# Optimization experiments

Hardware: AMD Instinct MI355X
Metric: run time of the kernel (lower is better)

## Reference

```python
import jax, jax.numpy as jnp
import numpy as np

N_NODES = 50000
N_EDGES = 800000
N_GRAPHS = 1000
D_NODE = 92
D_EDGE = 41
D_HID = 128
D_OUT = 1


def _glorot(key, shape):
    fan_in, fan_out = shape[1], shape[0]
    lim = jnp.sqrt(6.0 / (fan_in + fan_out))
    return jax.random.uniform(key, shape, jnp.float32, -lim, lim)


def setup_inputs() -> dict:
    key = jax.random.key(0)
    ks = jax.random.split(key, 16)
    x = jax.random.normal(ks[0], (N_NODES, D_NODE), jnp.float32)
    edge_index = jax.random.randint(ks[1], (2, N_EDGES), 0, N_NODES, jnp.int64)
    edge_attr = jax.random.uniform(ks[2], (N_EDGES, D_EDGE), jnp.float32)
    batch = jnp.sort(jax.random.randint(ks[3], (N_NODES,), 0, N_GRAPHS, jnp.int64))
    z_in = 2 * D_HID + D_EDGE  # CGConv concat dim
    return {
        "x": x, "edge_index": edge_index, "edge_attr": edge_attr, "batch": batch,
        "W_node": _glorot(ks[4], (D_HID, D_NODE)), "b_node": jnp.zeros((D_HID,), jnp.float32),
        "Wf1": _glorot(ks[5], (D_HID, z_in)), "bf1": jnp.zeros((D_HID,), jnp.float32),
        "Ws1": _glorot(ks[6], (D_HID, z_in)), "bs1": jnp.zeros((D_HID,), jnp.float32),
        "Wf2": _glorot(ks[7], (D_HID, z_in)), "bf2": jnp.zeros((D_HID,), jnp.float32),
        "Ws2": _glorot(ks[8], (D_HID, z_in)), "bs2": jnp.zeros((D_HID,), jnp.float32),
        "W1": _glorot(ks[9], (D_HID, D_HID)), "b1": jnp.zeros((D_HID,), jnp.float32),
        "W2": _glorot(ks[10], (D_OUT, D_HID)), "b2": jnp.zeros((D_OUT,), jnp.float32),
    }


def _cgconv(h, src, dst, edge_attr, Wf, bf, Ws, bs):
    # PyG CGConv: z_ij = [x_i, x_j, e_ij]; msg = sigmoid(lin_f(z)) * softplus(lin_s(z))
    # aggr='add' at target i; residual: out = x + aggr
    z = jnp.concatenate([h[dst], h[src], edge_attr], axis=1)  # [E, 2*D_HID + D_EDGE]
    msg = jax.nn.sigmoid(z @ Wf.T + bf) * jax.nn.softplus(z @ Ws.T + bs)  # [E, D_HID]
    agg = jax.ops.segment_sum(msg, dst, num_segments=N_NODES)
    return h + agg


def reference(x, edge_index, edge_attr, batch,
              W_node, b_node, Wf1, bf1, Ws1, bs1, Wf2, bf2, Ws2, bs2,
              W1, b1, W2, b2):
    src, dst = edge_index[0], edge_index[1]  # message flows j(src) -> i(dst)
    h = jax.nn.leaky_relu(x @ W_node.T + b_node)
    h = jax.nn.leaky_relu(_cgconv(h, src, dst, edge_attr, Wf1, bf1, Ws1, bs1))
    atom_embs = jax.nn.leaky_relu(_cgconv(h, src, dst, edge_attr, Wf2, bf2, Ws2, bs2))
    pooled = jax.ops.segment_sum(atom_embs, batch, num_segments=N_GRAPHS)  # [G, D_HID]
    norm = jnp.maximum(jnp.linalg.norm(pooled, axis=1, keepdims=True), 1e-12)
    g = pooled / norm
    g = jax.nn.leaky_relu(g @ W1.T + b1)
    out = g @ W2.T + b2
    return (out, atom_embs)
```

## Files before the change

kernel.cpp:

```cpp
#include <hip/hip_runtime.h>
#include <math.h>

#define NN 50000
#define NE 800000
#define NG 1000
#define DN 92
#define DE 41
#define DH 128

typedef float f32x4 __attribute__((ext_vector_type(4)));
typedef short s16x8 __attribute__((ext_vector_type(8)));
typedef float f32x4u __attribute__((ext_vector_type(4), aligned(4)));

#define OFF_A     ((size_t)0)
#define OFF_ABF   ((size_t)6400000)
#define OFF_PI    ((size_t)9600000)
#define OFF_PJ    ((size_t)16000000)
#define OFF_WCATB ((size_t)22400000)
#define OFF_WTE   ((size_t)22465536)
#define OFF_POOL  ((size_t)22481920)
#define OFF_CNT   ((size_t)22609920)
#define OFF_CUR   ((size_t)22659920)
#define OFF_SE    ((size_t)22709920)
#define OFF_SDST  ((size_t)24309920)

__device__ __forceinline__ float leaky(float x) { return x > 0.f ? x : 0.01f * x; }
__device__ __forceinline__ ushort f2bf(float x) {
    uint u = __float_as_uint(x);
    return (ushort)((u + 0x7fffu + ((u >> 16) & 1u)) >> 16);
}
__device__ __forceinline__ float bflo(uint u) { return __uint_as_float(u << 16); }
__device__ __forceinline__ float bfhi(uint u) { return __uint_as_float(u & 0xffff0000u); }

__device__ __forceinline__ float gate(float f, float s) {
    float sg = 1.f / (1.f + __expf(-f));
    float sp = fmaxf(s, 0.f) + __logf(1.f + __expf(-fabsf(s)));
    return sg * sp;
}

__device__ __forceinline__ int xcd_swz(int bid, int nbid) {
    int cpx = nbid >> 3;
    return (bid & 7) * cpx + (bid >> 3);
}

__device__ __forceinline__ s16x8 pack8(const float* v) {
    union { uint u[4]; s16x8 s; } r;
#pragma unroll
    for (int p = 0; p < 4; p++)
        asm("v_cvt_pk_bf16_f32 %0, %1, %2" : "=v"(r.u[p]) : "v"(v[2 * p]), "v"(v[2 * p + 1]));
    return r.s;
}
__device__ __forceinline__ uint cvtpk1(float a, float b) {
    uint r;
    asm("v_cvt_pk_bf16_f32 %0, %1, %2" : "=v"(r) : "v"(a), "v"(b));
    return r;
}

__global__ __launch_bounds__(128) void k_node_embed(const float* __restrict__ x,
        const float* __restrict__ Wn, const float* __restrict__ bn,
        float* __restrict__ A, ushort* __restrict__ Abf) {
    __shared__ __align__(16) float xs[16 * DN];
    const int n0 = blockIdx.x * 16;
    const int t = threadIdx.x;
    const float4* xg = (const float4*)(x + (size_t)n0 * DN);
    float4* xs4 = (float4*)xs;
    for (int i = t; i < 16 * DN / 4; i += 128) xs4[i] = xg[i];
    __syncthreads();
    const int o = t;
    float acc[16];
#pragma unroll
    for (int n = 0; n < 16; n++) acc[n] = 0.f;
    const float4* Wr = (const float4*)(Wn + (size_t)o * DN);
    for (int kk = 0; kk < DN / 4; kk++) {
        float4 w = Wr[kk];
#pragma unroll
        for (int n = 0; n < 16; n++) {
            float4 a = ((const float4*)(xs + n * DN))[kk];
            acc[n] = fmaf(w.x, a.x, acc[n]);
            acc[n] = fmaf(w.y, a.y, acc[n]);
            acc[n] = fmaf(w.z, a.z, acc[n]);
            acc[n] = fmaf(w.w, a.w, acc[n]);
        }
    }
    float b = bn[o];
#pragma unroll
    for (int n = 0; n < 16; n++) {
        float v = leaky(acc[n] + b);
        A[(size_t)(n0 + n) * DH + o] = v;
        Abf[(size_t)(n0 + n) * DH + o] = f2bf(v);
    }
}

__global__ __launch_bounds__(128) void k_pack_wcatb(const float* __restrict__ Wf1,
        const float* __restrict__ Ws1, const float* __restrict__ Wf2,
        const float* __restrict__ Ws2, ushort* __restrict__ Wcatb) {
    int b = blockIdx.x;
    int l = b >> 9, row = b & 511;
    int cb = row >> 7, o = row & 127;
    const float* src;
    if (l == 0) src = (cb < 2) ? Wf1 : Ws1;
    else        src = (cb < 2) ? Wf2 : Ws2;
    int koff = (cb & 1) * 128;
    Wcatb[(size_t)b * 128 + threadIdx.x] = f2bf(src[(size_t)o * 297 + koff + threadIdx.x]);
}

__global__ __launch_bounds__(64) void k_pack_wte(const float* __restrict__ Wf1,
        const float* __restrict__ Ws1, const float* __restrict__ Wf2,
        const float* __restrict__ Ws2, ushort* __restrict__ Wte) {
    int n = blockIdx.x, layer = blockIdx.y, k = threadIdx.x;
    int c = n >> 1, g = n & 1;
    const float* W = layer ? (g ? Ws2 : Wf2) : (g ? Ws1 : Wf1);
    float v = (k < DE) ? W[(size_t)c * 297 + 256 + k] : 0.f;
    Wte[((size_t)(layer * 256 + n)) * 64 + k] = f2bf(v);
}

__global__ __launch_bounds__(256) void k_hist(const int* __restrict__ ei,
        int* __restrict__ cnt) {
    int e = blockIdx.x * 256 + threadIdx.x;
    atomicAdd(&cnt[ei[NE + e]], 1);
}

__global__ __launch_bounds__(1024) void k_scan(const int* __restrict__ cnt,
        int* __restrict__ cur) {
    __shared__ int part[1024];
    const int t = threadIdx.x;
    const int lo = t * 49, hi = min(lo + 49, NN);
    int s = 0;
    for (int i = lo; i < hi; i++) s += cnt[i];
    part[t] = s;
    __syncthreads();
    for (int off = 1; off < 1024; off <<= 1) {
        int u = (t >= off) ? part[t - off] : 0;
        __syncthreads();
        part[t] += u;
        __syncthreads();
    }
    int run = part[t] - s;
    for (int i = lo; i < hi; i++) { int c = cnt[i]; cur[i] = run; run += c; }
}

__global__ __launch_bounds__(256) void k_scatter(const int* __restrict__ ei,
        int* __restrict__ cur, uint2* __restrict__ se, int* __restrict__ sdst) {
    int e = blockIdx.x * 256 + threadIdx.x;
    int src = ei[e], dst = ei[NE + e];
    int pos = atomicAdd(&cur[dst], 1);
    se[pos] = make_uint2((uint)src, (uint)e);
    sdst[pos] = dst;
}

__global__ __launch_bounds__(256) void k_gemm_P2(const ushort* __restrict__ Abf,
        const ushort* __restrict__ Wcatb, const float* __restrict__ bf,
        const float* __restrict__ bs, ushort* __restrict__ Pi,
        ushort* __restrict__ Pj) {
    __shared__ ushort Alds[32 * 136];
    __shared__ ushort OTi[32 * 264];
    __shared__ ushort OTj[32 * 264];
    const int n0 = blockIdx.x * 32;
    const int t = threadIdx.x;
    const int cb = t >> 6, l = t & 63, m16 = l & 15, g = l >> 4;

    const uint4* Ag = (const uint4*)Abf;
#pragma unroll
    for (int p = 0; p < 2; p++) {
        int row = (t >> 4) + p * 16;
        int node = n0 + row;
        uint4 v = make_uint4(0u, 0u, 0u, 0u);
        if (node < NN) v = Ag[(size_t)node * 16 + (t & 15)];
        *(uint4*)(Alds + row * 136 + (t & 15) * 8) = v;
    }
    __syncthreads();

    const ushort* Bw = Wcatb + (size_t)cb * 128 * 128;
    f32x4 acc[2][8];
#pragma unroll
    for (int mt = 0; mt < 2; mt++)
#pragma unroll
        for (int nt = 0; nt < 8; nt++) acc[mt][nt] = (f32x4){0.f, 0.f, 0.f, 0.f};

    for (int ks = 0; ks < 4; ks++) {
        s16x8 bfr[8];
#pragma unroll
        for (int nt = 0; nt < 8; nt++)
            bfr[nt] = *(const s16x8*)(Bw + ((size_t)(nt * 16 + m16)) * 128 + ks * 32 + g * 8);
        s16x8 afr[2];
#pragma unroll
        for (int mt = 0; mt < 2; mt++)
            afr[mt] = *(const s16x8*)(Alds + (mt * 16 + m16) * 136 + ks * 32 + g * 8);
#pragma unroll
        for (int mt = 0; mt < 2; mt++)
#pragma unroll
            for (int nt = 0; nt < 8; nt++)
                acc[mt][nt] = __builtin_amdgcn_mfma_f32_16x16x32_bf16(
                    afr[mt], bfr[nt], acc[mt][nt], 0, 0, 0);
    }

    float bias[8];
#pragma unroll
    for (int nt = 0; nt < 8; nt++) bias[nt] = 0.f;
    if (cb == 0) {
#pragma unroll
        for (int nt = 0; nt < 8; nt++) bias[nt] = bf[nt * 16 + m16];
    } else if (cb == 2) {
#pragma unroll
        for (int nt = 0; nt < 8; nt++) bias[nt] = bs[nt * 16 + m16];
    }
    ushort* OT = (cb & 1) ? OTj : OTi;
    const int sel = cb >> 1;
#pragma unroll
    for (int mt = 0; mt < 2; mt++)
#pragma unroll
        for (int nt = 0; nt < 8; nt++)
#pragma unroll
            for (int r = 0; r < 4; r++)
                OT[(mt * 16 + g * 4 + r) * 264 + (nt * 16 + m16) * 2 + sel] =
                    f2bf(acc[mt][nt][r] + bias[nt]);
    __syncthreads();
#pragma unroll
    for (int p = 0; p < 4; p++) {
        int idx = t + p * 256;
        int row = idx >> 5, col8 = idx & 31;
        int node = n0 + row;
        if (node < NN) {
            *(uint4*)(Pi + (size_t)node * 256 + col8 * 8) = *(const uint4*)(OTi + row * 264 + col8 * 8);
            *(uint4*)(Pj + (size_t)node * 256 + col8 * 8) = *(const uint4*)(OTj + row * 264 + col8 * 8);
        }
    }
}

__global__ __launch_bounds__(256) void k_edge(const ushort* __restrict__ Pi,
        const ushort* __restrict__ Pj, const uint2* __restrict__ se,
        const int* __restrict__ sdst, const float* __restrict__ ea,
        const ushort* __restrict__ Wte, float* __restrict__ A) {
    __shared__ ushort Elds[32 * 264];
    const int t = threadIdx.x, w = t >> 6, l = t & 63;
    const int bid = xcd_swz(blockIdx.x, gridDim.x);
    const int e0 = bid * 32;
    const int m16 = l & 15, g = l >> 4;

    s16x8 bt[4][2];
#pragma unroll
    for (int nt = 0; nt < 4; nt++)
#pragma unroll
        for (int ks = 0; ks < 2; ks++)
            bt[nt][ks] = *(const s16x8*)(Wte + ((size_t)(w * 64 + nt * 16 + m16)) * 64 + ks * 32 + g * 8);

    s16x8 at[2][2];
#pragma unroll
    for (int mt = 0; mt < 2; mt++) {
        uint2 s2 = se[e0 + mt * 16 + m16];
        const float* row = ea + (size_t)s2.y * DE;
        f32x4u q0 = *(const f32x4u*)(row + g * 8);
        f32x4u q1 = *(const f32x4u*)(row + g * 8 + 4);
        float v0[8] = {q0.x, q0.y, q0.z, q0.w, q1.x, q1.y, q1.z, q1.w};
        at[mt][0] = pack8(v0);
        float v1[8] = {0.f, 0.f, 0.f, 0.f, 0.f, 0.f, 0.f, 0.f};
        if (g == 0) {
            f32x4u q2 = *(const f32x4u*)(row + 32);
            f32x4u q3 = *(const f32x4u*)(row + 36);
            v1[0] = q2.x; v1[1] = q2.y; v1[2] = q2.z; v1[3] = q2.w;
            v1[4] = q3.x; v1[5] = q3.y; v1[6] = q3.z; v1[7] = q3.w;
        } else if (g == 1) {
            v1[0] = row[40];
        }
        at[mt][1] = pack8(v1);
    }

    f32x4 acc[2][4];
#pragma unroll
    for (int mt = 0; mt < 2; mt++)
#pragma unroll
        for (int nt = 0; nt < 4; nt++)
            acc[mt][nt] = (f32x4){0.f, 0.f, 0.f, 0.f};
#pragma unroll
    for (int ks = 0; ks < 2; ks++)
#pragma unroll
        for (int mt = 0; mt < 2; mt++)
#pragma unroll
            for (int nt = 0; nt < 4; nt++)
                acc[mt][nt] = __builtin_amdgcn_mfma_f32_16x16x32_bf16(
                    at[mt][ks], bt[nt][ks], acc[mt][nt], 0, 0, 0);

#pragma unroll
    for (int mt = 0; mt < 2; mt++)
#pragma unroll
        for (int nt = 0; nt < 4; nt++) {
            uint u01 = cvtpk1(acc[mt][nt][0], acc[mt][nt][1]);
            uint u23 = cvtpk1(acc[mt][nt][2], acc[mt][nt][3]);
            const int col = w * 64 + nt * 16 + m16;
            const int r0 = mt * 16 + g * 4;
            Elds[(r0 + 0) * 264 + col] = (ushort)u01;
            Elds[(r0 + 1) * 264 + col] = (ushort)(u01 >> 16);
            Elds[(r0 + 2) * 264 + col] = (ushort)u23;
            Elds[(r0 + 3) * 264 + col] = (ushort)(u23 >> 16);
        }
    __syncthreads();

    const uint* PiU = (const uint*)Pi;
    const uint* PjU = (const uint*)Pj;
    const uint* ElU = (const uint*)Elds;
    const int base = e0 + w * 8;
    uint mysrc = se[base + (l & 7)].x;
    int  mydst = sdst[base + (l & 7)];
    int dsts[8];
    float msg0[8], msg1[8];
#pragma unroll
    for (int i = 0; i < 8; i++) {
        const int src = __builtin_amdgcn_readlane((int)mysrc, i);
        const int dst = __builtin_amdgcn_readlane(mydst, i);
        dsts[i] = dst;
        const uint* pjb = PjU + (size_t)src * 128;
        const uint* pib = PiU + (size_t)dst * 128;
        uint pj0 = pjb[l],      pj1 = pjb[64 + l];
        uint pi0 = pib[l],      pi1 = pib[64 + l];
        uint ev0 = ElU[(w * 8 + i) * 132 + l];
        uint ev1 = ElU[(w * 8 + i) * 132 + 64 + l];
        float f0 = bflo(pi0) + bflo(pj0) + bflo(ev0);
        float s0 = bfhi(pi0) + bfhi(pj0) + bfhi(ev0);
        float f1 = bflo(pi1) + bflo(pj1) + bflo(ev1);
        float s1 = bfhi(pi1) + bfhi(pj1) + bfhi(ev1);
        msg0[i] = gate(f0, s0);
        msg1[i] = gate(f1, s1);
    }
    float c0 = msg0[0], c1 = msg1[0];
    int dprev = dsts[0];
#pragma unroll
    for (int i = 1; i < 8; i++) {
        if (dsts[i] == dprev) { c0 += msg0[i]; c1 += msg1[i]; }
        else {
            atomicAdd(A + (size_t)dprev * DH + l, c0);
            atomicAdd(A + (size_t)dprev * DH + 64 + l, c1);
            c0 = msg0[i]; c1 = msg1[i]; dprev = dsts[i];
        }
    }
    atomicAdd(A + (size_t)dprev * DH + l, c0);
    atomicAdd(A + (size_t)dprev * DH + 64 + l, c1);
}

__global__ __launch_bounds__(256) void k_act(float* __restrict__ A,
        ushort* __restrict__ Abf) {
    int i = blockIdx.x * 256 + threadIdx.x;
    float4* A4 = (float4*)A;
    float4 v = A4[i];
    v.x = leaky(v.x); v.y = leaky(v.y); v.z = leaky(v.z); v.w = leaky(v.w);
    A4[i] = v;
    ((uint2*)Abf)[i] = make_uint2(cvtpk1(v.x, v.y), cvtpk1(v.z, v.w));
}

__global__ __launch_bounds__(256) void k_finalize(const float* __restrict__ A,
        const int* __restrict__ batch, float* __restrict__ embs,
        float* __restrict__ pooled) {
    int idx = blockIdx.x * 256 + threadIdx.x;
    int n = idx >> 7, o = idx & 127;
    float v = leaky(A[idx]);
    embs[idx] = v;
    atomicAdd(pooled + (size_t)batch[n] * DH + o, v);
}

__global__ __launch_bounds__(128) void k_head(const float* __restrict__ pooled,
        const float* __restrict__ W1, const float* __restrict__ b1,
        const float* __restrict__ W2, const float* __restrict__ b2,
        float* __restrict__ out) {
    __shared__ __align__(16) float gl[128];
    __shared__ float red[2];
    const int g = blockIdx.x, o = threadIdx.x;
    const int l = o & 63, wid = o >> 6;
    float p = pooled[(size_t)g * DH + o];
    float v = p * p;
#pragma unroll
    for (int off = 32; off >= 1; off >>= 1) v += __shfl_xor(v, off);
    if (l == 0) red[wid] = v;
    __syncthreads();
    float nrm = fmaxf(sqrtf(red[0] + red[1]), 1e-12f);
    float gv = p / nrm;
    gl[o] = gv;
    __syncthreads();
    float gm = b1[o];
    const float4* Wr = (const float4*)(W1 + (size_t)o * DH);
    const float4* gl4 = (const float4*)gl;
    for (int kk = 0; kk < 32; kk++) {
        float4 w = Wr[kk]; float4 a = gl4[kk];
        gm = fmaf(w.x, a.x, gm); gm = fmaf(w.y, a.y, gm);
        gm = fmaf(w.z, a.z, gm); gm = fmaf(w.w, a.w, gm);
    }
    gm = leaky(gm);
    float c = gm * W2[o];
#pragma unroll
    for (int off = 32; off >= 1; off >>= 1) c += __shfl_xor(c, off);
    __syncthreads();
    if (l == 0) red[wid] = c;
    __syncthreads();
    if (o == 0) out[g] = red[0] + red[1] + b2[0];
}

extern "C" void kernel_launch(void* const* d_in, const int* in_sizes, int n_in,
                              void* d_out, int out_size, void* d_ws, size_t ws_size,
                              hipStream_t stream) {
    const float* x    = (const float*)d_in[0];
    const int*   ei   = (const int*)d_in[1];
    const float* ea   = (const float*)d_in[2];
    const int*   batch= (const int*)d_in[3];
    const float* Wn   = (const float*)d_in[4];
    const float* bn   = (const float*)d_in[5];
    const float* Wf1  = (const float*)d_in[6];
    const float* bf1  = (const float*)d_in[7];
    const float* Ws1  = (const float*)d_in[8];
    const float* bs1  = (const float*)d_in[9];
    const float* Wf2  = (const float*)d_in[10];
    const float* bf2  = (const float*)d_in[11];
    const float* Ws2  = (const float*)d_in[12];
    const float* bs2  = (const float*)d_in[13];
    const float* W1   = (const float*)d_in[14];
    const float* b1   = (const float*)d_in[15];
    const float* W2   = (const float*)d_in[16];
    const float* b2   = (const float*)d_in[17];

    float* ws      = (float*)d_ws;
    float*  A      = ws + OFF_A;
    ushort* Abf    = (ushort*)(ws + OFF_ABF);
    ushort* Pi     = (ushort*)(ws + OFF_PI);
    ushort* Pj     = (ushort*)(ws + OFF_PJ);
    ushort* Wcatb  = (ushort*)(ws + OFF_WCATB);
    ushort* Wte    = (ushort*)(ws + OFF_WTE);
    float*  pooled = ws + OFF_POOL;
    int*    cnt    = (int*)(ws + OFF_CNT);
    int*    cur    = (int*)(ws + OFF_CUR);
    uint2*  se     = (uint2*)(ws + OFF_SE);
    int*    sdst   = (int*)(ws + OFF_SDST);
    float* out     = (float*)d_out;
    float* embs    = out + NG;

    hipMemsetAsync(pooled, 0, (size_t)NG * DH * sizeof(float), stream);
    hipMemsetAsync(cnt, 0, (size_t)NN * sizeof(int), stream);
    k_pack_wcatb<<<1024, 128, 0, stream>>>(Wf1, Ws1, Wf2, Ws2, Wcatb);
    k_pack_wte<<<dim3(256, 2), 64, 0, stream>>>(Wf1, Ws1, Wf2, Ws2, Wte);
    k_node_embed<<<NN / 16, 128, 0, stream>>>(x, Wn, bn, A, Abf);

    k_hist<<<NE / 256, 256, 0, stream>>>(ei, cnt);
    k_scan<<<1, 1024, 0, stream>>>(cnt, cur);
    k_scatter<<<NE / 256, 256, 0, stream>>>(ei, cur, se, sdst);

    k_gemm_P2<<<(NN + 31) / 32, 256, 0, stream>>>(Abf, Wcatb, bf1, bs1, Pi, Pj);
    k_edge<<<NE / 32, 256, 0, stream>>>(Pi, Pj, se, sdst, ea, Wte, A);
    k_act<<<(NN * DH / 4) / 256, 256, 0, stream>>>(A, Abf);

    k_gemm_P2<<<(NN + 31) / 32, 256, 0, stream>>>(Abf, Wcatb + (size_t)512 * 128, bf2, bs2, Pi, Pj);
    k_edge<<<NE / 32, 256, 0, stream>>>(Pi, Pj, se, sdst, ea, Wte + (size_t)256 * 64, A);

    k_finalize<<<NN * DH / 256, 256, 0, stream>>>(A, batch, embs, pooled);
    k_head<<<NG, 128, 0, stream>>>(pooled, W1, b1, W2, b2, out);
}
```

Baseline: 695.6 us.

## Switch projections and edge GEMM to fp16 and dedupe Pi loads per destination

Changes the stored node projections, edge-weight tile and edge MFMA from bf16 to fp16, then sums the three terms with packed fp16 adds instead of unpacking to fp32. The edge loop now issues all source-row gathers first and reloads the destination-row projection only when the sorted destination changes. This removes redundant Pi gathers and conversion ALU work. The cost is lower dynamic range, so large projection values could overflow fp16.

```diff
diff --git a/kernel.cpp b/kernel.cpp
--- a/kernel.cpp
+++ b/kernel.cpp
@@ -10,6 +10,8 @@
 
 typedef float f32x4 __attribute__((ext_vector_type(4)));
 typedef short s16x8 __attribute__((ext_vector_type(8)));
+typedef __fp16 f16x2 __attribute__((ext_vector_type(2)));
+typedef __fp16 f16x8 __attribute__((ext_vector_type(8)));
 typedef float f32x4u __attribute__((ext_vector_type(4), aligned(4)));
 
 #define OFF_A     ((size_t)0)
@@ -29,8 +31,16 @@
     uint u = __float_as_uint(x);
     return (ushort)((u + 0x7fffu + ((u >> 16) & 1u)) >> 16);
 }
-__device__ __forceinline__ float bflo(uint u) { return __uint_as_float(u << 16); }
-__device__ __forceinline__ float bfhi(uint u) { return __uint_as_float(u & 0xffff0000u); }
+__device__ __forceinline__ ushort f2h(float x) {
+    union { __fp16 h; ushort u; } c;
+    c.h = (__fp16)x;
+    return c.u;
+}
+__device__ __forceinline__ f16x2 u2h(uint u) {
+    union { uint u; f16x2 h; } c;
+    c.u = u;
+    return c.h;
+}
 
 __device__ __forceinline__ float gate(float f, float s) {
     float sg = 1.f / (1.f + __expf(-f));
@@ -43,12 +53,17 @@
     return (bid & 7) * cpx + (bid >> 3);
 }
 
-__device__ __forceinline__ s16x8 pack8(const float* v) {
-    union { uint u[4]; s16x8 s; } r;
+__device__ __forceinline__ f16x8 pack8h(const float* v) {
+    union { f16x2 h[4]; f16x8 s; } r;
 #pragma unroll
     for (int p = 0; p < 4; p++)
-        asm("v_cvt_pk_bf16_f32 %0, %1, %2" : "=v"(r.u[p]) : "v"(v[2 * p]), "v"(v[2 * p + 1]));
+        r.h[p] = __builtin_amdgcn_cvt_pkrtz(v[2 * p], v[2 * p + 1]);
     return r.s;
+}
+__device__ __forceinline__ uint pkh1(float a, float b) {
+    union { f16x2 h; uint u; } c;
+    c.h = __builtin_amdgcn_cvt_pkrtz(a, b);
+    return c.u;
 }
 __device__ __forceinline__ uint cvtpk1(float a, float b) {
     uint r;
@@ -111,7 +126,7 @@
     int c = n >> 1, g = n & 1;
     const float* W = layer ? (g ? Ws2 : Wf2) : (g ? Ws1 : Wf1);
     float v = (k < DE) ? W[(size_t)c * 297 + 256 + k] : 0.f;
-    Wte[((size_t)(layer * 256 + n)) * 64 + k] = f2bf(v);
+    Wte[((size_t)(layer * 256 + n)) * 64 + k] = f2h(v);
 }
 
 __global__ __launch_bounds__(256) void k_hist(const int* __restrict__ ei,
@@ -213,7 +228,7 @@
 #pragma unroll
             for (int r = 0; r < 4; r++)
                 OT[(mt * 16 + g * 4 + r) * 264 + (nt * 16 + m16) * 2 + sel] =
-                    f2bf(acc[mt][nt][r] + bias[nt]);
+                    f2h(acc[mt][nt][r] + bias[nt]);
     __syncthreads();
 #pragma unroll
     for (int p = 0; p < 4; p++) {
@@ -237,14 +252,14 @@
     const int e0 = bid * 32;
     const int m16 = l & 15, g = l >> 4;
 
-    s16x8 bt[4][2];
+    f16x8 bt[4][2];
 #pragma unroll
     for (int nt = 0; nt < 4; nt++)
 #pragma unroll
         for (int ks = 0; ks < 2; ks++)
-            bt[nt][ks] = *(const s16x8*)(Wte + ((size_t)(w * 64 + nt * 16 + m16)) * 64 + ks * 32 + g * 8);
-
-    s16x8 at[2][2];
+            bt[nt][ks] = *(const f16x8*)(Wte + ((size_t)(w * 64 + nt * 16 + m16)) * 64 + ks * 32 + g * 8);
+
+    f16x8 at[2][2];
 #pragma unroll
     for (int mt = 0; mt < 2; mt++) {
         uint2 s2 = se[e0 + mt * 16 + m16];
@@ -252,7 +267,7 @@
         f32x4u q0 = *(const f32x4u*)(row + g * 8);
         f32x4u q1 = *(const f32x4u*)(row + g * 8 + 4);
         float v0[8] = {q0.x, q0.y, q0.z, q0.w, q1.x, q1.y, q1.z, q1.w};
-        at[mt][0] = pack8(v0);
+        at[mt][0] = pack8h(v0);
         float v1[8] = {0.f, 0.f, 0.f, 0.f, 0.f, 0.f, 0.f, 0.f};
         if (g == 0) {
             f32x4u q2 = *(const f32x4u*)(row + 32);
@@ -262,7 +277,7 @@
         } else if (g == 1) {
             v1[0] = row[40];
         }
-        at[mt][1] = pack8(v1);
+        at[mt][1] = pack8h(v1);
     }
 
     f32x4 acc[2][4];
@@ -277,15 +292,15 @@
         for (int mt = 0; mt < 2; mt++)
 #pragma unroll
             for (int nt = 0; nt < 4; nt++)
-                acc[mt][nt] = __builtin_amdgcn_mfma_f32_16x16x32_bf16(
+                acc[mt][nt] = __builtin_amdgcn_mfma_f32_16x16x32_f16(
                     at[mt][ks], bt[nt][ks], acc[mt][nt], 0, 0, 0);
 
 #pragma unroll
     for (int mt = 0; mt < 2; mt++)
 #pragma unroll
         for (int nt = 0; nt < 4; nt++) {
-            uint u01 = cvtpk1(acc[mt][nt][0], acc[mt][nt][1]);
-            uint u23 = cvtpk1(acc[mt][nt][2], acc[mt][nt][3]);
+            uint u01 = pkh1(acc[mt][nt][0], acc[mt][nt][1]);
+            uint u23 = pkh1(acc[mt][nt][2], acc[mt][nt][3]);
             const int col = w * 64 + nt * 16 + m16;
             const int r0 = mt * 16 + g * 4;
             Elds[(r0 + 0) * 264 + col] = (ushort)u01;
@@ -302,24 +317,33 @@
     uint mysrc = se[base + (l & 7)].x;
     int  mydst = sdst[base + (l & 7)];
     int dsts[8];
-    float msg0[8], msg1[8];
+    uint pj0a[8], pj1a[8];
 #pragma unroll
     for (int i = 0; i < 8; i++) {
         const int src = __builtin_amdgcn_readlane((int)mysrc, i);
-        const int dst = __builtin_amdgcn_readlane(mydst, i);
-        dsts[i] = dst;
+        dsts[i] = __builtin_amdgcn_readlane(mydst, i);
         const uint* pjb = PjU + (size_t)src * 128;
-        const uint* pib = PiU + (size_t)dst * 128;
-        uint pj0 = pjb[l],      pj1 = pjb[64 + l];
-        uint pi0 = pib[l],      pi1 = pib[64 + l];
+        pj0a[i] = pjb[l];
+        pj1a[i] = pjb[64 + l];
+    }
+    int dcur = dsts[0];
+    const uint* pib0 = PiU + (size_t)dcur * 128;
+    uint pi0 = pib0[l], pi1 = pib0[64 + l];
+    float msg0[8], msg1[8];
+#pragma unroll
+    for (int i = 0; i < 8; i++) {
+        if (dsts[i] != dcur) {
+            dcur = dsts[i];
+            const uint* pb = PiU + (size_t)dcur * 128;
+            pi0 = pb[l];
+            pi1 = pb[64 + l];
+        }
         uint ev0 = ElU[(w * 8 + i) * 132 + l];
         uint ev1 = ElU[(w * 8 + i) * 132 + 64 + l];
-        float f0 = bflo(pi0) + bflo(pj0) + bflo(ev0);
-        float s0 = bfhi(pi0) + bfhi(pj0) + bfhi(ev0);
-        float f1 = bflo(pi1) + bflo(pj1) + bflo(ev1);
-        float s1 = bfhi(pi1) + bfhi(pj1) + bfhi(ev1);
-        msg0[i] = gate(f0, s0);
-        msg1[i] = gate(f1, s1);
+        f16x2 t0 = u2h(pi0) + u2h(pj0a[i]) + u2h(ev0);
+        f16x2 t1 = u2h(pi1) + u2h(pj1a[i]) + u2h(ev1);
+        msg0[i] = gate((float)t0.x, (float)t0.y);
+        msg1[i] = gate((float)t1.x, (float)t1.y);
     }
     float c0 = msg0[0], c1 = msg1[0];
     int dprev = dsts[0];
```

Result: no change. 706.7 us (+1.6%).
